# Kernel tuning notes

Measured on AMD Instinct MI355X. Metric: run time of the kernel, lower is better.

The kernel has to match this reference:

```python
import jax, jax.numpy as jnp
import numpy as np

N_NODES = 100000
N_EDGES = 1600000
IN_CH = 128
OUT_CH = 64


def setup_inputs() -> dict:
    key = jax.random.key(0)
    k1, k2, k3 = jax.random.split(key, 3)
    x = jax.random.normal(k1, (N_NODES, IN_CH), dtype=jnp.float32)
    edge_index = jax.random.randint(k2, (2, N_EDGES), 0, N_NODES, dtype=jnp.int64)
    # Glorot-style init for the GCN weight, zero bias (PyG defaults)
    W = jax.random.normal(k3, (IN_CH, OUT_CH), dtype=jnp.float32) * (1.0 / np.sqrt(IN_CH))
    b = jnp.zeros((OUT_CH,), dtype=jnp.float32)
    return {"x": x, "edge_index": edge_index, "W": W, "b": b}


def reference(x, edge_index, W, b):
    n = x.shape[0]
    # add self loops (GCNConv default add_self_loops=True)
    loop = jnp.arange(n, dtype=edge_index.dtype)
    row = jnp.concatenate([edge_index[0], loop])  # source
    col = jnp.concatenate([edge_index[1], loop])  # target
    # symmetric degree normalization on augmented graph
    deg = jax.ops.segment_sum(jnp.ones_like(col, dtype=x.dtype), col, num_segments=n)
    dinv = jnp.where(deg > 0, jax.lax.rsqrt(deg), 0.0)
    norm = dinv[row] * dinv[col]  # [E+N]
    # linear transform first (out_channels < in_channels), then gather-scale-scatter
    h = x @ W  # [N, OUT]
    msgs = h[row] * norm[:, None]  # [E+N, OUT]
    out = jax.ops.segment_sum(msgs, col, num_segments=n)  # [N, OUT]
    return out + b
```

## Files before the change

### kernel.cpp

```cpp
#include <hip/hip_runtime.h>
#include <hip/hip_bf16.h>


#define IN_CH 128
#define OUT_CH 64
#define BSHIFT 7
#define BNODES 128
#define MAX_NB 800
#define CH_EDGES 7168
#define PSTRIDE 4096
#define SLOTS 32
#define SORT_CAP (BNODES * SLOTS)
#define OVSTRIDE 512
#define XSTR 136

typedef short bf16x8 __attribute__((ext_vector_type(8)));
typedef float f32x4  __attribute__((ext_vector_type(4)));

__device__ __forceinline__ unsigned short f2b(float f) {
    unsigned int u = __float_as_uint(f);
    return (unsigned short)((u + 0x7FFFu + ((u >> 16) & 1u)) >> 16);
}

__device__ __forceinline__ float blo(unsigned u) { return __uint_as_float(u << 16); }
__device__ __forceinline__ float bhi(unsigned u) { return __uint_as_float(u & 0xFFFF0000u); }

__global__ __launch_bounds__(256) void wprep_kernel(const float* __restrict__ W,
                                                    unsigned short* __restrict__ wbt,
                                                    int* __restrict__ cursor,
                                                    int NB) {
    int t = blockIdx.x * 256 + threadIdx.x;
    int k = t >> 6, nn = t & 63;
    wbt[nn * IN_CH + k] = f2b(W[t]);
    if (t < NB) cursor[t] = t * PSTRIDE;
}

__global__ __launch_bounds__(1024) void place_kernel(const int* __restrict__ row,
                                                     const int* __restrict__ col,
                                                     int* __restrict__ cursor,
                                                     int* __restrict__ pairs,
                                                     int E, int NB) {
    __shared__ int h[MAX_NB];
    int tid = threadIdx.x;
    for (int i = tid; i < NB; i += 1024) h[i] = 0;
    __syncthreads();
    int e0 = blockIdx.x * CH_EDGES;
    #pragma unroll
    for (int r1 = 0; r1 < CH_EDGES / 1024; ++r1) {
        int e = e0 + r1 * 1024 + tid;
        if (e < E) atomicAdd(&h[col[e] >> BSHIFT], 1);
    }
    __syncthreads();
    for (int i = tid; i < NB; i += 1024) {
        int c = h[i];
        if (c) h[i] = atomicAdd(&cursor[i], c);
    }
    __syncthreads();
    #pragma unroll
    for (int r2 = 0; r2 < CH_EDGES / 1024; ++r2) {
        int e = e0 + r2 * 1024 + tid;
        if (e < E) {
            int c = col[e];
            int b = c >> BSHIFT;
            int pos = atomicAdd(&h[b], 1);
            pairs[pos] = row[e] | ((c & (BNODES - 1)) << 17);
        }
    }
}

__global__ __launch_bounds__(256) void bucket_sort_kernel(
    const int* __restrict__ cursor_end, const int* __restrict__ pairs,
    int* __restrict__ csr, int* __restrict__ ovpairs, int* __restrict__ ovcnt,
    unsigned char* __restrict__ degb, float* __restrict__ dinv, int n)
{
    __shared__ int cnt[BNODES];
    __shared__ int cur[BNODES];
    __shared__ int sorted[SORT_CAP];
    __shared__ int ovl[OVSTRIDE];
    __shared__ int ovc;

    int b = blockIdx.x, tid = threadIdx.x;
    int node0 = b << BSHIFT;
    int nodeCnt = min(BNODES, n - node0);
    int s0 = b * PSTRIDE;
    int m  = cursor_end[b] - s0;

    if (tid < BNODES) { cnt[tid] = 0; cur[tid] = 0; }
    if (tid == 0) ovc = 0;
    __syncthreads();
    for (int e = tid; e < m; e += 256) atomicAdd(&cnt[pairs[s0 + e] >> 17], 1);
    #pragma unroll
    for (int i = 0; i < SORT_CAP / 256; ++i) sorted[tid + i * 256] = n;
    __syncthreads();
    if (tid < nodeCnt) {
        int d = cnt[tid];
        degb[node0 + tid] = (unsigned char)min(d, 255);
        dinv[node0 + tid] = rsqrtf((float)(d + 1));
    }
    __syncthreads();
    for (int e = tid; e < m; e += 256) {
        int p   = pairs[s0 + e];
        int lc  = p >> 17;
        int pos = atomicAdd(&cur[lc], 1);
        if (pos < SLOTS) sorted[lc * SLOTS + pos] = p & 0x1FFFF;
        else {
            int o = atomicAdd(&ovc, 1);
            if (o < OVSTRIDE) ovl[o] = p;
        }
    }
    __syncthreads();
    {
        int base = node0 * SLOTS;
        #pragma unroll
        for (int i = 0; i < SORT_CAP / 256; ++i)
            csr[base + tid + i * 256] = sorted[tid + i * 256];
    }
    int oc = min(ovc, OVSTRIDE);
    if (tid == 0) ovcnt[b] = oc;
    for (int i = tid; i < oc; i += 256) ovpairs[b * OVSTRIDE + i] = ovl[i];
}

__global__ __launch_bounds__(256) void gemm_kernel(
    const float* __restrict__ x, const unsigned short* __restrict__ wbt,
    const float* __restrict__ dinv, unsigned short* __restrict__ hpb, int n)
{
    __shared__ __align__(16) unsigned short xl[64 * XSTR];
    __shared__ __align__(16) unsigned short wl[64 * XSTR];

    int tid  = threadIdx.x;
    int row0 = blockIdx.x * 64;

    {
        const uint4* src = (const uint4*)wbt;
        #pragma unroll
        for (int i = 0; i < 4; ++i) {
            int flat = tid + i * 256;
            int nn = flat >> 4, c = flat & 15;
            *(uint4*)(wl + nn * XSTR + c * 8) = src[flat];
        }
    }
    #pragma unroll
    for (int i = 0; i < 4; ++i) {
        int r  = (tid >> 4) + i * 16;
        int c  = tid & 15;
        int gr = row0 + r;
        float4 v0 = make_float4(0.f,0.f,0.f,0.f), v1 = v0;
        float d = 0.f;
        if (gr < n) {
            d = dinv[gr];
            const float4* xr = (const float4*)(x + (size_t)gr * IN_CH);
            v0 = xr[c * 2]; v1 = xr[c * 2 + 1];
        }
        uint4 p;
        p.x = ((unsigned)f2b(v0.y * d) << 16) | f2b(v0.x * d);
        p.y = ((unsigned)f2b(v0.w * d) << 16) | f2b(v0.z * d);
        p.z = ((unsigned)f2b(v1.y * d) << 16) | f2b(v1.x * d);
        p.w = ((unsigned)f2b(v1.w * d) << 16) | f2b(v1.z * d);
        *(uint4*)(xl + r * XSTR + c * 8) = p;
    }
    __syncthreads();

    int lane = tid & 63, w = tid >> 6;
    int mrow = lane & 15;
    int g    = lane >> 4;

    f32x4 acc0 = {0,0,0,0}, acc1 = {0,0,0,0}, acc2 = {0,0,0,0}, acc3 = {0,0,0,0};
    const unsigned short* xbase = xl + (w * 16 + mrow) * XSTR + g * 8;
    const unsigned short* wbase = wl + mrow * XSTR + g * 8;

    #pragma unroll
    for (int k4 = 0; k4 < 4; ++k4) {
        bf16x8 a  = *(const bf16x8*)(xbase + k4 * 32);
        bf16x8 b0 = *(const bf16x8*)(wbase +             k4 * 32);
        bf16x8 b1 = *(const bf16x8*)(wbase + 16 * XSTR + k4 * 32);
        bf16x8 b2 = *(const bf16x8*)(wbase + 32 * XSTR + k4 * 32);
        bf16x8 b3 = *(const bf16x8*)(wbase + 48 * XSTR + k4 * 32);
        acc0 = __builtin_amdgcn_mfma_f32_16x16x32_bf16(a, b0, acc0, 0, 0, 0);
        acc1 = __builtin_amdgcn_mfma_f32_16x16x32_bf16(a, b1, acc1, 0, 0, 0);
        acc2 = __builtin_amdgcn_mfma_f32_16x16x32_bf16(a, b2, acc2, 0, 0, 0);
        acc3 = __builtin_amdgcn_mfma_f32_16x16x32_bf16(a, b3, acc3, 0, 0, 0);
    }
    __syncthreads();

    {
        int cm = g * 4;
        #pragma unroll
        for (int r = 0; r < 4; ++r) {
            unsigned short* crow = xl + (w * 16 + cm + r) * XSTR + mrow;
            crow[ 0] = f2b(acc0[r]);
            crow[16] = f2b(acc1[r]);
            crow[32] = f2b(acc2[r]);
            crow[48] = f2b(acc3[r]);
        }
    }
    __syncthreads();
    #pragma unroll
    for (int i = 0; i < 2; ++i) {
        int flat = tid + i * 256;
        int r = flat >> 3, c = flat & 7;
        int gr = row0 + r;
        if (gr <= n) {
            uint4 v = *(const uint4*)(xl + r * XSTR + c * 8);
            *(uint4*)(hpb + (size_t)gr * OUT_CH + c * 8) = v;
        }
    }
}

__global__ __launch_bounds__(256) void aggregate_kernel(
    const int* __restrict__ csr, const int* __restrict__ ovpairs,
    const int* __restrict__ ovcnt, const unsigned char* __restrict__ degb,
    const unsigned short* __restrict__ hpb, const float* __restrict__ dinv,
    const float* __restrict__ bias, float* __restrict__ out, int n)
{
    int pw   = (blockIdx.x * 256 + threadIdx.x) >> 6;
    int lane = threadIdx.x & 63;
    int A = 2 * pw, B = A + 1;
    if (A >= n) return;
    int e = lane >> 3;
    int c = lane & 7;

    const uint4* hp16 = (const uint4*)hpb;

    int iv = csr[A * SLOTS + lane];
    float2 dd = ((const float2*)dinv)[pw];
    unsigned short ds = ((const unsigned short*)degb)[pw];
    int bno = A >> BSHIFT;
    int oc  = ovcnt[bno];
    int srow = (lane & 8) ? B : A;
    uint4 sv = hp16[(unsigned)(srow * 8 + c)];

    int degA = ds & 255, degB = ds >> 8;
    int rA = (min(degA, SLOTS) + 7) >> 3;
    int rB = (min(degB, SLOTS) + 7) >> 3;

    float axl=0.f,axh=0.f, ayl=0.f,ayh=0.f, azl=0.f,azh=0.f, awl=0.f,awh=0.f;
    float bxl=0.f,bxh=0.f, byl=0.f,byh=0.f, bzl=0.f,bzh=0.f, bwl=0.f,bwh=0.f;

    #define GATHER(ACC_XL,ACC_XH,ACC_YL,ACC_YH,ACC_ZL,ACC_ZH,ACC_WL,ACC_WH, SRC) \
        { int r_ = __shfl(iv, (SRC));                                            \
          uint4 v_ = hp16[(unsigned)(r_ * 8 + c)];                               \
          ACC_XL += blo(v_.x); ACC_XH += bhi(v_.x);                              \
          ACC_YL += blo(v_.y); ACC_YH += bhi(v_.y);                              \
          ACC_ZL += blo(v_.z); ACC_ZH += bhi(v_.z);                              \
          ACC_WL += blo(v_.w); ACC_WH += bhi(v_.w); }

    if (rA > 0) GATHER(axl,axh,ayl,ayh,azl,azh,awl,awh,      e)
    if (rB > 0) GATHER(bxl,bxh,byl,byh,bzl,bzh,bwl,bwh, 32 + e)
    if (rA > 1) GATHER(axl,axh,ayl,ayh,azl,azh,awl,awh,  8 + e)
    if (rB > 1) GATHER(bxl,bxh,byl,byh,bzl,bzh,bwl,bwh, 40 + e)
    if (rA > 2) GATHER(axl,axh,ayl,ayh,azl,azh,awl,awh, 16 + e)
    if (rB > 2) GATHER(bxl,bxh,byl,byh,bzl,bzh,bwl,bwh, 48 + e)
    if (rA > 3) GATHER(axl,axh,ayl,ayh,azl,azh,awl,awh, 24 + e)
    if (rB > 3) GATHER(bxl,bxh,byl,byh,bzl,bzh,bwl,bwh, 56 + e)
    #undef GATHER

    if (oc > 0) {
        const int* op = ovpairs + bno * OVSTRIDE;
        for (int i = 0; i < oc; ++i) {
            int p    = op[i];
            int node = (bno << BSHIFT) + (p >> 17);
            if (node == A || node == B) {
                uint4 v = hp16[(unsigned)((p & 0x1FFFF) * 8 + c)];
                if (e == 0) {
                    if (node == A) {
                        axl += blo(v.x); axh += bhi(v.x); ayl += blo(v.y); ayh += bhi(v.y);
                        azl += blo(v.z); azh += bhi(v.z); awl += blo(v.w); awh += bhi(v.w);
                    } else {
                        bxl += blo(v.x); bxh += bhi(v.x); byl += blo(v.y); byh += bhi(v.y);
                        bzl += blo(v.z); bzh += bhi(v.z); bwl += blo(v.w); bwh += bhi(v.w);
                    }
                }
            }
        }
    }

    #pragma unroll
    for (int m = 8; m < 64; m <<= 1) {
        axl += __shfl_xor(axl, m); axh += __shfl_xor(axh, m);
        ayl += __shfl_xor(ayl, m); ayh += __shfl_xor(ayh, m);
        azl += __shfl_xor(azl, m); azh += __shfl_xor(azh, m);
        awl += __shfl_xor(awl, m); awh += __shfl_xor(awh, m);
        bxl += __shfl_xor(bxl, m); bxh += __shfl_xor(bxh, m);
        byl += __shfl_xor(byl, m); byh += __shfl_xor(byh, m);
        bzl += __shfl_xor(bzl, m); bzh += __shfl_xor(bzh, m);
        bwl += __shfl_xor(bwl, m); bwh += __shfl_xor(bwh, m);
    }

    if (lane < 16) {
        int   node = srow;
        float d    = (lane & 8) ? dd.y : dd.x;
        float sxl, sxh, syl, syh, szl, szh, swl, swh;
        if (lane & 8) { sxl=bxl; sxh=bxh; syl=byl; syh=byh; szl=bzl; szh=bzh; swl=bwl; swh=bwh; }
        else          { sxl=axl; sxh=axh; syl=ayl; syh=ayh; szl=azl; szh=azh; swl=awl; swh=awh; }
        sxl += blo(sv.x); sxh += bhi(sv.x);
        syl += blo(sv.y); syh += bhi(sv.y);
        szl += blo(sv.z); szh += bhi(sv.z);
        swl += blo(sv.w); swh += bhi(sv.w);
        float4 b0 = ((const float4*)bias)[2 * c];
        float4 b1 = ((const float4*)bias)[2 * c + 1];
        float4 o0, o1;
        o0.x = fmaf(d, sxl, b0.x); o0.y = fmaf(d, sxh, b0.y);
        o0.z = fmaf(d, syl, b0.z); o0.w = fmaf(d, syh, b0.w);
        o1.x = fmaf(d, szl, b1.x); o1.y = fmaf(d, szh, b1.y);
        o1.z = fmaf(d, swl, b1.z); o1.w = fmaf(d, swh, b1.w);
        float* op = out + (size_t)node * OUT_CH + c * 8;
        *(float4*)op       = o0;
        *(float4*)(op + 4) = o1;
    }
}

extern "C" void kernel_launch(void* const* d_in, const int* in_sizes, int n_in,
                              void* d_out, int out_size, void* d_ws, size_t ws_size,
                              hipStream_t stream) {
    const float* x  = (const float*)d_in[0];
    const int*   ei = (const int*)d_in[1];
    const float* W  = (const float*)d_in[2];
    const float* b  = (const float*)d_in[3];
    float*       out = (float*)d_out;

    int n = in_sizes[0] / IN_CH;
    int E = in_sizes[1] / 2;
    const int* row = ei;
    const int* col = ei + E;

    int NB   = (n + BNODES - 1) >> BSHIFT;
    int NBLK = (E + CH_EDGES - 1) / CH_EDGES;

    char* ws = (char*)d_ws;
    int*   cursor       = (int*)ws;   ws += (size_t)NB * 4;
    int*   ovcnt        = (int*)ws;   ws += (size_t)NB * 4;
    float* dinv         = (float*)ws; ws += (size_t)n * 4;
    unsigned char* degb = (unsigned char*)ws; ws += (size_t)(n + 2) & ~1ull; ws = (char*)(((uintptr_t)ws + 255) & ~(uintptr_t)255);
    unsigned short* wbt = (unsigned short*)ws; ws += (size_t)IN_CH * OUT_CH * 2;
    ws = (char*)(((uintptr_t)ws + 255) & ~(uintptr_t)255);
    int*   pairs        = (int*)ws;   ws += (size_t)NB * PSTRIDE * 4;
    int*   ovpairs      = (int*)ws;   ws += (size_t)NB * OVSTRIDE * 4;
    int*   csr          = (int*)ws;   ws += (size_t)NB * BNODES * SLOTS * 4;
    unsigned short* hpb = (unsigned short*)ws;

    wprep_kernel      <<<(IN_CH * OUT_CH) / 256, 256, 0, stream>>>(W, wbt, cursor, NB);
    place_kernel      <<<NBLK, 1024, 0, stream>>>(row, col, cursor, pairs, E, NB);
    bucket_sort_kernel<<<NB, 256, 0, stream>>>(cursor, pairs, csr, ovpairs, ovcnt, degb, dinv, n);
    gemm_kernel       <<<(n + 63) / 64, 256, 0, stream>>>(x, wbt, dinv, hpb, n);
    aggregate_kernel  <<<(n / 2 * 64 + 255) / 256, 256, 0, stream>>>(csr, ovpairs, ovcnt, degb, hpb, dinv, b, out, n);
}
```

Baseline: 168.4 us.

## Vectorize edge placement and CSR copy; use one wave per node in aggregate

```diff
diff --git a/kernel.cpp b/kernel.cpp
--- a/kernel.cpp
+++ b/kernel.cpp
@@ -7,7 +7,7 @@
 #define BSHIFT 7
 #define BNODES 128
 #define MAX_NB 800
-#define CH_EDGES 7168
+#define CH_EDGES 8192
 #define PSTRIDE 4096
 #define SLOTS 32
 #define SORT_CAP (BNODES * SLOTS)
@@ -46,9 +46,15 @@
     __syncthreads();
     int e0 = blockIdx.x * CH_EDGES;
     #pragma unroll
-    for (int r1 = 0; r1 < CH_EDGES / 1024; ++r1) {
-        int e = e0 + r1 * 1024 + tid;
-        if (e < E) atomicAdd(&h[col[e] >> BSHIFT], 1);
+    for (int r1 = 0; r1 < CH_EDGES / 4096; ++r1) {
+        int e = e0 + (r1 * 1024 + tid) * 4;
+        if (e < E) {
+            int4 c4 = *(const int4*)(col + e);
+            atomicAdd(&h[c4.x >> BSHIFT], 1);
+            atomicAdd(&h[c4.y >> BSHIFT], 1);
+            atomicAdd(&h[c4.z >> BSHIFT], 1);
+            atomicAdd(&h[c4.w >> BSHIFT], 1);
+        }
     }
     __syncthreads();
     for (int i = tid; i < NB; i += 1024) {
@@ -57,13 +63,21 @@
     }
     __syncthreads();
     #pragma unroll
-    for (int r2 = 0; r2 < CH_EDGES / 1024; ++r2) {
-        int e = e0 + r2 * 1024 + tid;
+    for (int r2 = 0; r2 < CH_EDGES / 4096; ++r2) {
+        int e = e0 + (r2 * 1024 + tid) * 4;
         if (e < E) {
-            int c = col[e];
-            int b = c >> BSHIFT;
-            int pos = atomicAdd(&h[b], 1);
-            pairs[pos] = row[e] | ((c & (BNODES - 1)) << 17);
+            int4 c4 = *(const int4*)(col + e);
+            int4 r4 = *(const int4*)(row + e);
+            int b0 = c4.x >> BSHIFT, b1 = c4.y >> BSHIFT;
+            int b2 = c4.z >> BSHIFT, b3 = c4.w >> BSHIFT;
+            int p0 = atomicAdd(&h[b0], 1);
+            pairs[p0] = r4.x | ((c4.x & (BNODES - 1)) << 17);
+            int p1 = atomicAdd(&h[b1], 1);
+            pairs[p1] = r4.y | ((c4.y & (BNODES - 1)) << 17);
+            int p2 = atomicAdd(&h[b2], 1);
+            pairs[p2] = r4.z | ((c4.z & (BNODES - 1)) << 17);
+            int p3 = atomicAdd(&h[b3], 1);
+            pairs[p3] = r4.w | ((c4.w & (BNODES - 1)) << 17);
         }
     }
 }
@@ -75,7 +89,7 @@
 {
     __shared__ int cnt[BNODES];
     __shared__ int cur[BNODES];
-    __shared__ int sorted[SORT_CAP];
+    __shared__ __align__(16) int sorted[SORT_CAP];
     __shared__ int ovl[OVSTRIDE];
     __shared__ int ovc;
 
@@ -110,10 +124,11 @@
     }
     __syncthreads();
     {
-        int base = node0 * SLOTS;
+        uint4* dst = (uint4*)(csr + node0 * SLOTS);
+        const uint4* src = (const uint4*)sorted;
         #pragma unroll
-        for (int i = 0; i < SORT_CAP / 256; ++i)
-            csr[base + tid + i * 256] = sorted[tid + i * 256];
+        for (int i = 0; i < SORT_CAP / 1024; ++i)
+            dst[tid + i * 256] = src[tid + i * 256];
     }
     int oc = min(ovc, OVSTRIDE);
     if (tid == 0) ovcnt[b] = oc;
@@ -212,46 +227,38 @@
     const unsigned short* __restrict__ hpb, const float* __restrict__ dinv,
     const float* __restrict__ bias, float* __restrict__ out, int n)
 {
-    int pw   = (blockIdx.x * 256 + threadIdx.x) >> 6;
+    int wid  = (blockIdx.x * 256 + threadIdx.x) >> 6;
     int lane = threadIdx.x & 63;
-    int A = 2 * pw, B = A + 1;
-    if (A >= n) return;
-    int e = lane >> 3;
-    int c = lane & 7;
+    if (wid >= n) return;
+    int e   = lane >> 3;
+    int c   = lane & 7;
+    int l31 = lane & 31;
 
     const uint4* hp16 = (const uint4*)hpb;
 
-    int iv = csr[A * SLOTS + lane];
-    float2 dd = ((const float2*)dinv)[pw];
-    unsigned short ds = ((const unsigned short*)degb)[pw];
-    int bno = A >> BSHIFT;
+    int iv = csr[wid * SLOTS + l31];
+    float d = dinv[wid];
+    int deg = degb[wid];
+    int bno = wid >> BSHIFT;
     int oc  = ovcnt[bno];
-    int srow = (lane & 8) ? B : A;
-    uint4 sv = hp16[(unsigned)(srow * 8 + c)];
-
-    int degA = ds & 255, degB = ds >> 8;
-    int rA = (min(degA, SLOTS) + 7) >> 3;
-    int rB = (min(degB, SLOTS) + 7) >> 3;
+    uint4 sv = hp16[(unsigned)(wid * 8 + c)];
+
+    int rnds = (min(deg, SLOTS) + 7) >> 3;
 
     float axl=0.f,axh=0.f, ayl=0.f,ayh=0.f, azl=0.f,azh=0.f, awl=0.f,awh=0.f;
-    float bxl=0.f,bxh=0.f, byl=0.f,byh=0.f, bzl=0.f,bzh=0.f, bwl=0.f,bwh=0.f;
-
-    #define GATHER(ACC_XL,ACC_XH,ACC_YL,ACC_YH,ACC_ZL,ACC_ZH,ACC_WL,ACC_WH, SRC) \
+
+    #define GATHER(SRC) \
         { int r_ = __shfl(iv, (SRC));                                            \
           uint4 v_ = hp16[(unsigned)(r_ * 8 + c)];                               \
-          ACC_XL += blo(v_.x); ACC_XH += bhi(v_.x);                              \
-          ACC_YL += blo(v_.y); ACC_YH += bhi(v_.y);                              \
-          ACC_ZL += blo(v_.z); ACC_ZH += bhi(v_.z);                              \
-          ACC_WL += blo(v_.w); ACC_WH += bhi(v_.w); }
-
-    if (rA > 0) GATHER(axl,axh,ayl,ayh,azl,azh,awl,awh,      e)
-    if (rB > 0) GATHER(bxl,bxh,byl,byh,bzl,bzh,bwl,bwh, 32 + e)
-    if (rA > 1) GATHER(axl,axh,ayl,ayh,azl,azh,awl,awh,  8 + e)
-    if (rB > 1) GATHER(bxl,bxh,byl,byh,bzl,bzh,bwl,bwh, 40 + e)
-    if (rA > 2) GATHER(axl,axh,ayl,ayh,azl,azh,awl,awh, 16 + e)
-    if (rB > 2) GATHER(bxl,bxh,byl,byh,bzl,bzh,bwl,bwh, 48 + e)
-    if (rA > 3) GATHER(axl,axh,ayl,ayh,azl,azh,awl,awh, 24 + e)
-    if (rB > 3) GATHER(bxl,bxh,byl,byh,bzl,bzh,bwl,bwh, 56 + e)
+          axl += blo(v_.x); axh += bhi(v_.x);                                    \
+          ayl += blo(v_.y); ayh += bhi(v_.y);                                    \
+          azl += blo(v_.z); azh += bhi(v_.z);                                    \
+          awl += blo(v_.w); awh += bhi(v_.w); }
+
+    if (rnds > 0) GATHER(     e)
+    if (rnds > 1) GATHER( 8 + e)
+    if (rnds > 2) GATHER(16 + e)
+    if (rnds > 3) GATHER(24 + e)
     #undef GATHER
 
     if (oc > 0) {
@@ -259,16 +266,11 @@
         for (int i = 0; i < oc; ++i) {
             int p    = op[i];
             int node = (bno << BSHIFT) + (p >> 17);
-            if (node == A || node == B) {
+            if (node == wid) {
                 uint4 v = hp16[(unsigned)((p & 0x1FFFF) * 8 + c)];
                 if (e == 0) {
-                    if (node == A) {
-                        axl += blo(v.x); axh += bhi(v.x); ayl += blo(v.y); ayh += bhi(v.y);
-                        azl += blo(v.z); azh += bhi(v.z); awl += blo(v.w); awh += bhi(v.w);
-                    } else {
-                        bxl += blo(v.x); bxh += bhi(v.x); byl += blo(v.y); byh += bhi(v.y);
-                        bzl += blo(v.z); bzh += bhi(v.z); bwl += blo(v.w); bwh += bhi(v.w);
-                    }
+                    axl += blo(v.x); axh += bhi(v.x); ayl += blo(v.y); ayh += bhi(v.y);
+                    azl += blo(v.z); azh += bhi(v.z); awl += blo(v.w); awh += bhi(v.w);
                 }
             }
         }
@@ -280,30 +282,21 @@
         ayl += __shfl_xor(ayl, m); ayh += __shfl_xor(ayh, m);
         azl += __shfl_xor(azl, m); azh += __shfl_xor(azh, m);
         awl += __shfl_xor(awl, m); awh += __shfl_xor(awh, m);
-        bxl += __shfl_xor(bxl, m); bxh += __shfl_xor(bxh, m);
-        byl += __shfl_xor(byl, m); byh += __shfl_xor(byh, m);
-        bzl += __shfl_xor(bzl, m); bzh += __shfl_xor(bzh, m);
-        bwl += __shfl_xor(bwl, m); bwh += __shfl_xor(bwh, m);
-    }
-
-    if (lane < 16) {
-        int   node = srow;
-        float d    = (lane & 8) ? dd.y : dd.x;
-        float sxl, sxh, syl, syh, szl, szh, swl, swh;
-        if (lane & 8) { sxl=bxl; sxh=bxh; syl=byl; syh=byh; szl=bzl; szh=bzh; swl=bwl; swh=bwh; }
-        else          { sxl=axl; sxh=axh; syl=ayl; syh=ayh; szl=azl; szh=azh; swl=awl; swh=awh; }
-        sxl += blo(sv.x); sxh += bhi(sv.x);
-        syl += blo(sv.y); syh += bhi(sv.y);
-        szl += blo(sv.z); szh += bhi(sv.z);
-        swl += blo(sv.w); swh += bhi(sv.w);
+    }
+
+    if (e == 0) {
+        axl += blo(sv.x); axh += bhi(sv.x);
+        ayl += blo(sv.y); ayh += bhi(sv.y);
+        azl += blo(sv.z); azh += bhi(sv.z);
+        awl += blo(sv.w); awh += bhi(sv.w);
         float4 b0 = ((const float4*)bias)[2 * c];
         float4 b1 = ((const float4*)bias)[2 * c + 1];
         float4 o0, o1;
-        o0.x = fmaf(d, sxl, b0.x); o0.y = fmaf(d, sxh, b0.y);
-        o0.z = fmaf(d, syl, b0.z); o0.w = fmaf(d, syh, b0.w);
-        o1.x = fmaf(d, szl, b1.x); o1.y = fmaf(d, szh, b1.y);
-        o1.z = fmaf(d, swl, b1.z); o1.w = fmaf(d, swh, b1.w);
-        float* op = out + (size_t)node * OUT_CH + c * 8;
+        o0.x = fmaf(d, axl, b0.x); o0.y = fmaf(d, axh, b0.y);
+        o0.z = fmaf(d, ayl, b0.z); o0.w = fmaf(d, ayh, b0.w);
+        o1.x = fmaf(d, azl, b1.x); o1.y = fmaf(d, azh, b1.y);
+        o1.z = fmaf(d, awl, b1.z); o1.w = fmaf(d, awh, b1.w);
+        float* op = out + (size_t)wid * OUT_CH + c * 8;
         *(float4*)op       = o0;
         *(float4*)(op + 4) = o1;
     }
@@ -342,5 +335,5 @@
     place_kernel      <<<NBLK, 1024, 0, stream>>>(row, col, cursor, pairs, E, NB);
     bucket_sort_kernel<<<NB, 256, 0, stream>>>(cursor, pairs, csr, ovpairs, ovcnt, degb, dinv, n);
     gemm_kernel       <<<(n + 63) / 64, 256, 0, stream>>>(x, wbt, dinv, hpb, n);
-    aggregate_kernel  <<<(n / 2 * 64 + 255) / 256, 256, 0, stream>>>(csr, ovpairs, ovcnt, degb, hpb, dinv, b, out, n);
-}
+    aggregate_kernel  <<<((size_t)n * 64 + 255) / 256, 256, 0, stream>>>(csr, ovpairs, ovcnt, degb, hpb, dinv, b, out, n);
+}
```

After: 170.8 us. About the same (+1.4%).
